# Optimization experiments

Measured on AMD Instinct MI355X. Metric: run time of the kernel, lower is better.

## Reference

```python
import jax, jax.numpy as jnp
import numpy as np

EPS = 1e-4


def setup_inputs() -> dict:
    key = jax.random.key(0)
    k1, k2, k3 = jax.random.split(key, 3)
    B, N = 1024, 8192
    src = jax.random.normal(k1, (B, 3, N), dtype=jnp.float32)
    rcs = jax.random.normal(k2, (B, 3, N), dtype=jnp.float32)
    weights = jax.random.uniform(k3, (B, N), dtype=jnp.float32)
    return {"src": src, "rcs": rcs, "weights": weights}


def reference(src, rcs, weights):
    # src, rcs: [B, 3, N]; weights: [B, N]
    B = src.shape[0]
    src_corres = src + rcs
    sum_w = jnp.sum(weights, axis=1, keepdims=True) + EPS          # [B,1]
    nw = weights / sum_w                                           # [B,N], sums ~1
    w = nw[:, None, :]                                             # [B,1,N]
    denom = jnp.sum(w, axis=2, keepdims=True) + EPS                # [B,1,1]
    src_mean = jnp.sum(src * w, axis=2, keepdims=True) / denom     # [B,3,1]
    corres_mean = jnp.sum(src_corres * w, axis=2, keepdims=True) / denom
    sc = src - src_mean                                            # [B,3,N]
    cc = src_corres - corres_mean                                  # [B,3,N]
    # weighted covariance: equals src_centered @ diag(nw) @ corres_centered^T
    cov = jnp.einsum('bin,bn,bjn->bij', sc, nw, cc)                # [B,3,3]
    u, s, vh = jnp.linalg.svd(cov, full_matrices=False)
    v = jnp.swapaxes(vh, 1, 2)
    ut = jnp.swapaxes(u, 1, 2)
    det = jnp.linalg.det(v @ ut)                                   # [B]
    d = jnp.concatenate(
        [jnp.ones((B, 2), dtype=src.dtype), det[:, None]], axis=1)  # [B,3]
    # r = v @ diag(d) @ u^T
    r = v @ (d[:, :, None] * ut)                                   # [B,3,3]
    t = corres_mean[..., 0] - jnp.einsum('bij,bj->bi', r, src_mean[..., 0])
    return (r, t)
```

## Files before the change

### kernel.cpp

```cpp
#include <hip/hip_runtime.h>
#include <math.h>

constexpr int N_ELEM = 8192;
constexpr int TPB    = 512;
constexpr int CHUNKS = N_ELEM / 4 / TPB;

__global__ __launch_bounds__(TPB) void gw_reduce_kernel(
    const float* __restrict__ src, const float* __restrict__ rcs,
    const float* __restrict__ wts, float* __restrict__ sums )
{
    const size_t b = blockIdx.x;
    const float4* w4 = (const float4*)(wts + b * (size_t)N_ELEM);
    const float4* x0 = (const float4*)(src + b * (size_t)(3 * N_ELEM));
    const float4* x1 = x0 + N_ELEM / 4;
    const float4* x2 = x0 + 2 * (N_ELEM / 4);
    const float4* r0 = (const float4*)(rcs + b * (size_t)(3 * N_ELEM));
    const float4* r1 = r0 + N_ELEM / 4;
    const float4* r2 = r0 + 2 * (N_ELEM / 4);

    float s[16];
#pragma unroll
    for (int k = 0; k < 16; ++k) s[k] = 0.f;

#pragma unroll
    for (int c = 0; c < CHUNKS; ++c) {
        const int idx = c * TPB + threadIdx.x;
        float4 wv = w4[idx];
        float4 a0 = x0[idx], a1 = x1[idx], a2 = x2[idx];
        float4 b0 = r0[idx], b1 = r1[idx], b2 = r2[idx];
        const float* wp = (const float*)&wv;
        const float* p0 = (const float*)&a0;
        const float* p1 = (const float*)&a1;
        const float* p2 = (const float*)&a2;
        const float* q0 = (const float*)&b0;
        const float* q1 = (const float*)&b1;
        const float* q2 = (const float*)&b2;
#pragma unroll
        for (int k = 0; k < 4; ++k) {
            const float w  = wp[k];
            const float X0 = p0[k], X1 = p1[k], X2 = p2[k];
            const float Y0 = X0 + q0[k], Y1 = X1 + q1[k], Y2 = X2 + q2[k];
            const float wX0 = w * X0, wX1 = w * X1, wX2 = w * X2;
            s[0]  += w;
            s[1]  += wX0;      s[2]  += wX1;      s[3]  += wX2;
            s[4]  += w * Y0;   s[5]  += w * Y1;   s[6]  += w * Y2;
            s[7]  += wX0 * Y0; s[8]  += wX0 * Y1; s[9]  += wX0 * Y2;
            s[10] += wX1 * Y0; s[11] += wX1 * Y1; s[12] += wX1 * Y2;
            s[13] += wX2 * Y0; s[14] += wX2 * Y1; s[15] += wX2 * Y2;
        }
    }

#pragma unroll
    for (int off = 32; off > 0; off >>= 1) {
#pragma unroll
        for (int k = 0; k < 16; ++k) s[k] += __shfl_down(s[k], off, 64);
    }

    __shared__ float lds[TPB / 64][16];
    const int wave = threadIdx.x >> 6;
    const int lane = threadIdx.x & 63;
    if (lane == 0) {
#pragma unroll
        for (int k = 0; k < 16; ++k) lds[wave][k] = s[k];
    }
    __syncthreads();
    if (threadIdx.x < 16) {
        float acc = 0.f;
#pragma unroll
        for (int wv = 0; wv < TPB / 64; ++wv) acc += lds[wv][threadIdx.x];
        sums[b * 16 + threadIdx.x] = acc;
    }
}

__global__ void gw_solve_kernel(const float* __restrict__ sums,
                                float* __restrict__ out, int B)
{
    const int b = blockIdx.x * blockDim.x + threadIdx.x;
    if (b >= B) return;
    const float* S = sums + (size_t)b * 16;

    const double EPS = 1e-4;
    const double Sw = S[0];
    double Sx[3] = {S[1], S[2], S[3]};
    double Sy[3] = {S[4], S[5], S[6]};

    const double sum_w = Sw + EPS;
    const double denom = Sw / sum_w + EPS;
    const double mscale = 1.0 / (sum_w * denom);
    double mx[3], my[3];
#pragma unroll
    for (int i = 0; i < 3; ++i) { mx[i] = Sx[i] * mscale; my[i] = Sy[i] * mscale; }

    double H[3][3];
#pragma unroll
    for (int i = 0; i < 3; ++i)
#pragma unroll
        for (int j = 0; j < 3; ++j) {
            const double Sxy = S[7 + 3 * i + j];
            H[i][j] = (Sxy - mx[i] * Sy[j] - my[j] * Sx[i] + mx[i] * my[j] * Sw) / sum_w;
        }

    double A[3][3];
#pragma unroll
    for (int i = 0; i < 3; ++i)
#pragma unroll
        for (int j = 0; j < 3; ++j)
            A[i][j] = H[0][i] * H[0][j] + H[1][i] * H[1][j] + H[2][i] * H[2][j];

    double V[3][3] = {{1, 0, 0}, {0, 1, 0}, {0, 0, 1}};

    for (int sweep = 0; sweep < 8; ++sweep) {
        const int PP[3] = {0, 0, 1}, QQ[3] = {1, 2, 2};
#pragma unroll
        for (int r = 0; r < 3; ++r) {
            const int p = PP[r], q = QQ[r];
            const double apq = A[p][q];
            if (fabs(apq) < 1e-300) continue;
            const double theta = (A[q][q] - A[p][p]) / (2.0 * apq);
            const double t = copysign(1.0, theta) / (fabs(theta) + sqrt(1.0 + theta * theta));
            const double c = 1.0 / sqrt(1.0 + t * t);
            const double sn = t * c;
            const double App = A[p][p], Aqq = A[q][q];
            A[p][p] = App - t * apq;
            A[q][q] = Aqq + t * apq;
            A[p][q] = A[q][p] = 0.0;
            const int k = 3 - p - q;
            const double Akp = A[k][p], Akq = A[k][q];
            A[k][p] = A[p][k] = c * Akp - sn * Akq;
            A[k][q] = A[q][k] = sn * Akp + c * Akq;
#pragma unroll
            for (int m = 0; m < 3; ++m) {
                const double Vmp = V[m][p], Vmq = V[m][q];
                V[m][p] = c * Vmp - sn * Vmq;
                V[m][q] = sn * Vmp + c * Vmq;
            }
        }
    }

    double ev[3] = {A[0][0], A[1][1], A[2][2]};
    int ord[3] = {0, 1, 2};
    if (ev[ord[0]] < ev[ord[1]]) { int tmp = ord[0]; ord[0] = ord[1]; ord[1] = tmp; }
    if (ev[ord[0]] < ev[ord[2]]) { int tmp = ord[0]; ord[0] = ord[2]; ord[2] = tmp; }
    if (ev[ord[1]] < ev[ord[2]]) { int tmp = ord[1]; ord[1] = ord[2]; ord[2] = tmp; }

    double Vs[3][3], Us[3][3], sig[3];
#pragma unroll
    for (int k = 0; k < 3; ++k) {
        const int c0 = ord[k];
        for (int m = 0; m < 3; ++m) Vs[m][k] = V[m][c0];
        double u0 = H[0][0] * Vs[0][k] + H[0][1] * Vs[1][k] + H[0][2] * Vs[2][k];
        double u1 = H[1][0] * Vs[0][k] + H[1][1] * Vs[1][k] + H[1][2] * Vs[2][k];
        double u2 = H[2][0] * Vs[0][k] + H[2][1] * Vs[1][k] + H[2][2] * Vs[2][k];
        const double nrm = sqrt(u0 * u0 + u1 * u1 + u2 * u2);
        sig[k] = nrm;
        const double inv = (nrm > 1e-150) ? 1.0 / nrm : 0.0;
        Us[0][k] = u0 * inv; Us[1][k] = u1 * inv; Us[2][k] = u2 * inv;
    }
    if (sig[2] <= 1e-8 * fmax(sig[0], 1e-300)) {
        double c0 = Us[1][0] * Us[2][1] - Us[2][0] * Us[1][1];
        double c1 = Us[2][0] * Us[0][1] - Us[0][0] * Us[2][1];
        double c2 = Us[0][0] * Us[1][1] - Us[1][0] * Us[0][1];
        const double n = sqrt(c0 * c0 + c1 * c1 + c2 * c2);
        const double inv = (n > 1e-150) ? 1.0 / n : 0.0;
        Us[0][2] = c0 * inv; Us[1][2] = c1 * inv; Us[2][2] = c2 * inv;
    }

    auto det3 = [](double M[3][3]) {
        return M[0][0] * (M[1][1] * M[2][2] - M[1][2] * M[2][1])
             - M[0][1] * (M[1][0] * M[2][2] - M[1][2] * M[2][0])
             + M[0][2] * (M[1][0] * M[2][1] - M[1][1] * M[2][0]);
    };
    const double d = (det3(Us) * det3(Vs) < 0.0) ? -1.0 : 1.0;

    double R[3][3];
#pragma unroll
    for (int i = 0; i < 3; ++i)
#pragma unroll
        for (int j = 0; j < 3; ++j)
            R[i][j] = Vs[i][0] * Us[j][0] + Vs[i][1] * Us[j][1] + d * Vs[i][2] * Us[j][2];

    float* outR = out + (size_t)b * 9;
    float* outT = out + (size_t)B * 9 + (size_t)b * 3;
#pragma unroll
    for (int i = 0; i < 3; ++i) {
#pragma unroll
        for (int j = 0; j < 3; ++j) outR[i * 3 + j] = (float)R[i][j];
        outT[i] = (float)(my[i] - (R[i][0] * mx[0] + R[i][1] * mx[1] + R[i][2] * mx[2]));
    }
}

extern "C" void kernel_launch(void* const* d_in, const int* in_sizes, int n_in,
                              void* d_out, int out_size, void* d_ws, size_t ws_size,
                              hipStream_t stream) {
    const float* src = (const float*)d_in[0];
    const float* rcs = (const float*)d_in[1];
    const float* wts = (const float*)d_in[2];
    float* out  = (float*)d_out;
    float* sums = (float*)d_ws;

    const int B = in_sizes[2] / N_ELEM;

    gw_reduce_kernel<<<B, TPB, 0, stream>>>(src, rcs, wts, sums);
    gw_solve_kernel<<<(B + 255) / 256, 256, 0, stream>>>(sums, out, B);
}
```

Before: 48.82 us.

## Fuse reduction and 3x3 SVD solve into one kernel in fp32

Merges the per-batch reduction kernel and the separate solve kernel, so thread 0 of each block runs the Jacobi SVD right after the block reduction. This removes the second launch and the workspace round trip. The solve also moves from double to float, Jacobi sweeps drop from 8 to 6, and launch bounds now request 8 blocks per CU. The risks are lower accuracy near degenerate covariances, and a serial tail per block where a single thread does the solve while the other waves sit idle.

```diff
diff --git a/kernel.cpp b/kernel.cpp
--- a/kernel.cpp
+++ b/kernel.cpp
@@ -5,9 +5,9 @@
 constexpr int TPB    = 512;
 constexpr int CHUNKS = N_ELEM / 4 / TPB;
 
-__global__ __launch_bounds__(TPB) void gw_reduce_kernel(
+__global__ __launch_bounds__(TPB, 8) void gw_fused_kernel(
     const float* __restrict__ src, const float* __restrict__ rcs,
-    const float* __restrict__ wts, float* __restrict__ sums )
+    const float* __restrict__ wts, float* __restrict__ out, int B)
 {
     const size_t b = blockIdx.x;
     const float4* w4 = (const float4*)(wts + b * (size_t)N_ELEM);
@@ -64,115 +64,111 @@
         for (int k = 0; k < 16; ++k) lds[wave][k] = s[k];
     }
     __syncthreads();
-    if (threadIdx.x < 16) {
+
+    if (threadIdx.x != 0) return;
+
+    float S[16];
+#pragma unroll
+    for (int k = 0; k < 16; ++k) {
         float acc = 0.f;
 #pragma unroll
-        for (int wv = 0; wv < TPB / 64; ++wv) acc += lds[wv][threadIdx.x];
-        sums[b * 16 + threadIdx.x] = acc;
+        for (int wv = 0; wv < TPB / 64; ++wv) acc += lds[wv][k];
+        S[k] = acc;
     }
-}
 
-__global__ void gw_solve_kernel(const float* __restrict__ sums,
-                                float* __restrict__ out, int B)
-{
-    const int b = blockIdx.x * blockDim.x + threadIdx.x;
-    if (b >= B) return;
-    const float* S = sums + (size_t)b * 16;
+    const float EPS = 1e-4f;
+    const float Sw = S[0];
+    float Sx[3] = {S[1], S[2], S[3]};
+    float Sy[3] = {S[4], S[5], S[6]};
 
-    const double EPS = 1e-4;
-    const double Sw = S[0];
-    double Sx[3] = {S[1], S[2], S[3]};
-    double Sy[3] = {S[4], S[5], S[6]};
-
-    const double sum_w = Sw + EPS;
-    const double denom = Sw / sum_w + EPS;
-    const double mscale = 1.0 / (sum_w * denom);
-    double mx[3], my[3];
+    const float sum_w = Sw + EPS;
+    const float denom = Sw / sum_w + EPS;
+    const float mscale = 1.0f / (sum_w * denom);
+    float mx[3], my[3];
 #pragma unroll
     for (int i = 0; i < 3; ++i) { mx[i] = Sx[i] * mscale; my[i] = Sy[i] * mscale; }
 
-    double H[3][3];
+    float H[3][3];
 #pragma unroll
     for (int i = 0; i < 3; ++i)
 #pragma unroll
         for (int j = 0; j < 3; ++j) {
-            const double Sxy = S[7 + 3 * i + j];
+            const float Sxy = S[7 + 3 * i + j];
             H[i][j] = (Sxy - mx[i] * Sy[j] - my[j] * Sx[i] + mx[i] * my[j] * Sw) / sum_w;
         }
 
-    double A[3][3];
+    float A[3][3];
 #pragma unroll
     for (int i = 0; i < 3; ++i)
 #pragma unroll
         for (int j = 0; j < 3; ++j)
             A[i][j] = H[0][i] * H[0][j] + H[1][i] * H[1][j] + H[2][i] * H[2][j];
 
-    double V[3][3] = {{1, 0, 0}, {0, 1, 0}, {0, 0, 1}};
+    float V[3][3] = {{1, 0, 0}, {0, 1, 0}, {0, 0, 1}};
 
-    for (int sweep = 0; sweep < 8; ++sweep) {
+    for (int sweep = 0; sweep < 6; ++sweep) {
         const int PP[3] = {0, 0, 1}, QQ[3] = {1, 2, 2};
 #pragma unroll
         for (int r = 0; r < 3; ++r) {
             const int p = PP[r], q = QQ[r];
-            const double apq = A[p][q];
-            if (fabs(apq) < 1e-300) continue;
-            const double theta = (A[q][q] - A[p][p]) / (2.0 * apq);
-            const double t = copysign(1.0, theta) / (fabs(theta) + sqrt(1.0 + theta * theta));
-            const double c = 1.0 / sqrt(1.0 + t * t);
-            const double sn = t * c;
-            const double App = A[p][p], Aqq = A[q][q];
-            A[p][p] = App - t * apq;
-            A[q][q] = Aqq + t * apq;
-            A[p][q] = A[q][p] = 0.0;
+            const float apq = A[p][q];
+            if (fabsf(apq) < 1e-30f) continue;
+            const float theta = (A[q][q] - A[p][p]) / (2.0f * apq);
+            const float t = copysignf(1.0f, theta) / (fabsf(theta) + sqrtf(1.0f + theta * theta));
+            const float c = 1.0f / sqrtf(1.0f + t * t);
+            const float sn = t * c;
+            A[p][p] = A[p][p] - t * apq;
+            A[q][q] = A[q][q] + t * apq;
+            A[p][q] = A[q][p] = 0.0f;
             const int k = 3 - p - q;
-            const double Akp = A[k][p], Akq = A[k][q];
+            const float Akp = A[k][p], Akq = A[k][q];
             A[k][p] = A[p][k] = c * Akp - sn * Akq;
             A[k][q] = A[q][k] = sn * Akp + c * Akq;
 #pragma unroll
             for (int m = 0; m < 3; ++m) {
-                const double Vmp = V[m][p], Vmq = V[m][q];
+                const float Vmp = V[m][p], Vmq = V[m][q];
                 V[m][p] = c * Vmp - sn * Vmq;
                 V[m][q] = sn * Vmp + c * Vmq;
             }
         }
     }
 
-    double ev[3] = {A[0][0], A[1][1], A[2][2]};
+    float ev[3] = {A[0][0], A[1][1], A[2][2]};
     int ord[3] = {0, 1, 2};
     if (ev[ord[0]] < ev[ord[1]]) { int tmp = ord[0]; ord[0] = ord[1]; ord[1] = tmp; }
     if (ev[ord[0]] < ev[ord[2]]) { int tmp = ord[0]; ord[0] = ord[2]; ord[2] = tmp; }
     if (ev[ord[1]] < ev[ord[2]]) { int tmp = ord[1]; ord[1] = ord[2]; ord[2] = tmp; }
 
-    double Vs[3][3], Us[3][3], sig[3];
+    float Vs[3][3], Us[3][3], sig[3];
 #pragma unroll
     for (int k = 0; k < 3; ++k) {
         const int c0 = ord[k];
         for (int m = 0; m < 3; ++m) Vs[m][k] = V[m][c0];
-        double u0 = H[0][0] * Vs[0][k] + H[0][1] * Vs[1][k] + H[0][2] * Vs[2][k];
-        double u1 = H[1][0] * Vs[0][k] + H[1][1] * Vs[1][k] + H[1][2] * Vs[2][k];
-        double u2 = H[2][0] * Vs[0][k] + H[2][1] * Vs[1][k] + H[2][2] * Vs[2][k];
-        const double nrm = sqrt(u0 * u0 + u1 * u1 + u2 * u2);
+        float u0 = H[0][0] * Vs[0][k] + H[0][1] * Vs[1][k] + H[0][2] * Vs[2][k];
+        float u1 = H[1][0] * Vs[0][k] + H[1][1] * Vs[1][k] + H[1][2] * Vs[2][k];
+        float u2 = H[2][0] * Vs[0][k] + H[2][1] * Vs[1][k] + H[2][2] * Vs[2][k];
+        const float nrm = sqrtf(u0 * u0 + u1 * u1 + u2 * u2);
         sig[k] = nrm;
-        const double inv = (nrm > 1e-150) ? 1.0 / nrm : 0.0;
+        const float inv = (nrm > 1e-30f) ? 1.0f / nrm : 0.0f;
         Us[0][k] = u0 * inv; Us[1][k] = u1 * inv; Us[2][k] = u2 * inv;
     }
-    if (sig[2] <= 1e-8 * fmax(sig[0], 1e-300)) {
-        double c0 = Us[1][0] * Us[2][1] - Us[2][0] * Us[1][1];
-        double c1 = Us[2][0] * Us[0][1] - Us[0][0] * Us[2][1];
-        double c2 = Us[0][0] * Us[1][1] - Us[1][0] * Us[0][1];
-        const double n = sqrt(c0 * c0 + c1 * c1 + c2 * c2);
-        const double inv = (n > 1e-150) ? 1.0 / n : 0.0;
+    if (sig[2] <= 1e-6f * fmaxf(sig[0], 1e-30f)) {
+        float c0 = Us[1][0] * Us[2][1] - Us[2][0] * Us[1][1];
+        float c1 = Us[2][0] * Us[0][1] - Us[0][0] * Us[2][1];
+        float c2 = Us[0][0] * Us[1][1] - Us[1][0] * Us[0][1];
+        const float n = sqrtf(c0 * c0 + c1 * c1 + c2 * c2);
+        const float inv = (n > 1e-30f) ? 1.0f / n : 0.0f;
         Us[0][2] = c0 * inv; Us[1][2] = c1 * inv; Us[2][2] = c2 * inv;
     }
 
-    auto det3 = [](double M[3][3]) {
+    auto det3 = [](float M[3][3]) {
         return M[0][0] * (M[1][1] * M[2][2] - M[1][2] * M[2][1])
              - M[0][1] * (M[1][0] * M[2][2] - M[1][2] * M[2][0])
              + M[0][2] * (M[1][0] * M[2][1] - M[1][1] * M[2][0]);
     };
-    const double d = (det3(Us) * det3(Vs) < 0.0) ? -1.0 : 1.0;
+    const float d = (det3(Us) * det3(Vs) < 0.0f) ? -1.0f : 1.0f;
 
-    double R[3][3];
+    float R[3][3];
 #pragma unroll
     for (int i = 0; i < 3; ++i)
 #pragma unroll
@@ -184,8 +180,8 @@
 #pragma unroll
     for (int i = 0; i < 3; ++i) {
 #pragma unroll
-        for (int j = 0; j < 3; ++j) outR[i * 3 + j] = (float)R[i][j];
-        outT[i] = (float)(my[i] - (R[i][0] * mx[0] + R[i][1] * mx[1] + R[i][2] * mx[2]));
+        for (int j = 0; j < 3; ++j) outR[i * 3 + j] = R[i][j];
+        outT[i] = my[i] - (R[i][0] * mx[0] + R[i][1] * mx[1] + R[i][2] * mx[2]);
     }
 }
 
@@ -195,11 +191,9 @@
     const float* src = (const float*)d_in[0];
     const float* rcs = (const float*)d_in[1];
     const float* wts = (const float*)d_in[2];
-    float* out  = (float*)d_out;
-    float* sums = (float*)d_ws;
+    float* out = (float*)d_out;
 
     const int B = in_sizes[2] / N_ELEM;
 
-    gw_reduce_kernel<<<B, TPB, 0, stream>>>(src, rcs, wts, sums);
-    gw_solve_kernel<<<(B + 255) / 256, 256, 0, stream>>>(sums, out, B);
+    gw_fused_kernel<<<B, TPB, 0, stream>>>(src, rcs, wts, out, B);
 }
```

After: 115.4 us. 136% more time.
